# Performance work log

Hardware: AMD Instinct MI355X
Metric: run time of the kernel (lower is better)

## Reference

```python
import jax, jax.numpy as jnp
import numpy as np

N = 100000
E = 1600000
D_FEAT = 64
D_HID = 64
T = 20
DT = 0.5


def setup_inputs() -> dict:
    key = jax.random.key(0)
    ks = jax.random.split(key, 12)
    inp = {
        "S0": jax.random.uniform(ks[0], (N,), dtype=jnp.float32),
        "I0": jax.random.uniform(ks[1], (N,), dtype=jnp.float32),
        "R0": jnp.zeros((N,), dtype=jnp.float32),
        "time_grid": jnp.arange(T, dtype=jnp.float32),
        "node_feat": jax.random.normal(ks[2], (N, D_FEAT), dtype=jnp.float32),
        "edge_index": jax.random.randint(ks[3], (2, E), 0, N, dtype=jnp.int64),
        "edge_weight": jax.random.uniform(ks[4], (E,), dtype=jnp.float32),
        "W_msg": jax.random.normal(ks[5], (D_FEAT + 1, D_HID), dtype=jnp.float32) * 0.1,
        "W_self": jax.random.normal(ks[6], (D_FEAT + 1, D_HID), dtype=jnp.float32) * 0.1,
        "b_h": jnp.zeros((D_HID,), dtype=jnp.float32),
        "w_beta": jax.random.normal(ks[7], (D_HID,), dtype=jnp.float32) * 0.1,
        "b_beta": jnp.zeros((1,), dtype=jnp.float32),
        "w_gamma": jax.random.normal(ks[8], (D_HID,), dtype=jnp.float32) * 0.1,
        "b_gamma": jnp.zeros((1,), dtype=jnp.float32),
    }
    return inp


def reference(S0, I0, R0, time_grid, node_feat, edge_index, edge_weight,
              W_msg, W_self, b_h, w_beta, b_beta, w_gamma, b_gamma):
    n = S0.shape[0]
    src = edge_index[0]
    dst = edge_index[1]

    def step(carry, _):
        S, I, R = carry
        # gnn block: x_in = [node_feat, I]  -> [N, d_feat+1]
        x_in = jnp.concatenate([node_feat, I[:, None]], axis=-1)
        # project first, then gather: (x_in @ W_msg)[src] is math-equivalent to x_in[src] @ W_msg
        msg = (x_in @ W_msg)[src] * edge_weight[:, None]          # [E, d_hid]
        agg = jax.ops.segment_sum(msg, dst, num_segments=n)       # [N, d_hid]
        h = jax.nn.relu(agg + x_in @ W_self + b_h)
        # param net: per-node beta/gamma
        beta = jax.nn.sigmoid(h @ w_beta + b_beta[0])             # [N]
        gamma = jax.nn.sigmoid(h @ w_gamma + b_gamma[0])          # [N]
        # edge scatter-add force
        force = jax.ops.segment_sum(edge_weight * I[src], dst, num_segments=n)
        force = jnp.clip(force, 0.0, 1000.0)
        inf = beta * S * force
        rec = gamma * I
        S = jnp.clip(S + (-inf) * DT, 0.0, 1.0)
        I = jnp.clip(I + (inf - rec) * DT, 0.0, 1.0)
        R = jnp.clip(R + rec * DT, 0.0, 1.0)
        return (S, I, R), (I, beta, gamma)

    (_, _, _), (I_seq, betas, gammas) = jax.lax.scan(
        step, (S0, I0, R0), None, length=time_grid.shape[0])
    return I_seq, betas[-1], gammas[-1]
```

## Files before the change

### kernel.cpp

```cpp
#include <hip/hip_runtime.h>
#include <hip/hip_fp16.h>
#include <cstdint>
#include <cstddef>

#define DT_F 0.5f
#define ELL_C 64
#define NBIN 768
#define BCAP 512
#define NSC 96

__global__ void detect_i64(const long long* __restrict__ ei, int E, int n,
                           int* __restrict__ flag) {
    __shared__ int ok;
    if (threadIdx.x == 0) ok = 1;
    __syncthreads();
    int m = E < 2048 ? E : 2048;
    for (int i = threadIdx.x; i < m; i += blockDim.x) {
        long long v = ei[i];
        if (v < 0 || v >= (long long)n) ok = 0;
    }
    __syncthreads();
    if (threadIdx.x == 0) flag[0] = ok;
}

__device__ __forceinline__ int ld_idx(const void* ei, size_t pos, int w64) {
    return w64 ? (int)((const long long*)ei)[pos] : ((const int*)ei)[pos];
}

__global__ void k_bin(const void* __restrict__ ei, const float* __restrict__ ew,
                      const int* __restrict__ flag, int E, int n,
                      int colbits, float scale,
                      int2* __restrict__ staging, int scap,
                      int* __restrict__ gcur,
                      int* __restrict__ cnt, uint32_t* __restrict__ ev) {
    __shared__ int2 bins[8][BCAP];
    __shared__ int bcnt[8];
    __shared__ int gbase[8];
    int tid = threadIdx.x;
    if (tid < 8) bcnt[tid] = 0;
    __syncthreads();
    int per = (E + NBIN - 1) / NBIN;
    int e0 = blockIdx.x * per;
    int e1 = e0 + per; if (e1 > E) e1 = E;
    int w64 = flag[0];
    for (int e = e0 + tid; e < e1; e += blockDim.x) {
        int d = ld_idx(ei, (size_t)E + e, w64);
        uint32_t w15 = (uint32_t)(ew[e] * scale + 0.5f);
        uint32_t sw = (w15 << colbits) | (uint32_t)ld_idx(ei, e, w64);
        int s = (int)(((long long)d * 8) / n);
        int p = atomicAdd(&bcnt[s], 1);
        if (p < BCAP) {
            bins[s][p] = make_int2(d, (int)sw);
        } else {
            int q = atomicAdd(&cnt[d], 1);
            if (q < ELL_C) ev[(size_t)d * ELL_C + q] = sw;
        }
    }
    __syncthreads();
    if (tid < 8) {
        int c = bcnt[tid]; if (c > BCAP) c = BCAP;
        bcnt[tid] = c;
        gbase[tid] = atomicAdd(&gcur[tid], c);
    }
    __syncthreads();
    for (int s = 0; s < 8; ++s) {
        int c = bcnt[s], gb = gbase[s];
        for (int i = tid; i < c; i += blockDim.x) {
            int pos = gb + i;
            if (pos < scap) {
                staging[(size_t)s * scap + pos] = bins[s][i];
            } else {
                int2 t = bins[s][i];
                int q = atomicAdd(&cnt[t.x], 1);
                if (q < ELL_C) ev[(size_t)t.x * ELL_C + q] = (uint32_t)t.y;
            }
        }
    }
}

__global__ void k_scatter(const int2* __restrict__ staging, int scap,
                          const int* __restrict__ gcur,
                          int* __restrict__ cnt, uint32_t* __restrict__ ev) {
    int s   = blockIdx.x & 7;
    int blk = blockIdx.x >> 3;
    int tot = gcur[s]; if (tot > scap) tot = scap;
    int per = (tot + NSC - 1) / NSC;
    int i0 = blk * per;
    int i1 = i0 + per; if (i1 > tot) i1 = tot;
    for (int i = i0 + (int)threadIdx.x; i < i1; i += blockDim.x) {
        int2 t = staging[(size_t)s * scap + i];
        int p = atomicAdd(&cnt[t.x], 1);
        if (p < ELL_C) ev[(size_t)t.x * ELL_C + p] = (uint32_t)t.y;
    }
}

__global__ void k_h16(const float* __restrict__ x, __half* __restrict__ y, int n) {
    int i = blockIdx.x * blockDim.x + threadIdx.x;
    if (i < n) y[i] = __float2half(x[i]);
}

__global__ void proj_tiled(const float* __restrict__ nf,
                           const float* __restrict__ Wm,
                           const float* __restrict__ Wsf,
                           const float* __restrict__ bh,
                           __half* __restrict__ PMh, float* __restrict__ HC,
                           int n) {
    __shared__ float sWmT[64 * 65];
    __shared__ float sWsT[64 * 65];
    __shared__ float sNf[64 * 68];
    for (int i = threadIdx.x; i < 64 * 64; i += 256) {
        int k = i >> 6, j = i & 63;
        sWmT[j * 65 + k] = Wm[i];
        sWsT[j * 65 + k] = Wsf[i];
    }
    int node0 = blockIdx.x * 64;
    for (int i = threadIdx.x; i < 64 * 64; i += 256) {
        int r = i >> 6, c = i & 63;
        if (node0 + r < n) sNf[r * 68 + c] = nf[(size_t)(node0 + r) * 64 + c];
    }
    __syncthreads();
    int w   = threadIdx.x >> 6;
    int j   = threadIdx.x & 63;
    float accm[16], accs[16];
#pragma unroll
    for (int ni = 0; ni < 16; ++ni) { accm[ni] = 0.f; accs[ni] = 0.f; }
    for (int kq = 0; kq < 16; ++kq) {
        int k = kq * 4;
        float wm0 = sWmT[j * 65 + k],     wm1 = sWmT[j * 65 + k + 1];
        float wm2 = sWmT[j * 65 + k + 2], wm3 = sWmT[j * 65 + k + 3];
        float ws0 = sWsT[j * 65 + k],     ws1 = sWsT[j * 65 + k + 1];
        float ws2 = sWsT[j * 65 + k + 2], ws3 = sWsT[j * 65 + k + 3];
#pragma unroll
        for (int ni = 0; ni < 16; ++ni) {
            float4 a = *(const float4*)&sNf[(w * 16 + ni) * 68 + k];
            accm[ni] = fmaf(a.w, wm3, fmaf(a.z, wm2, fmaf(a.y, wm1, fmaf(a.x, wm0, accm[ni]))));
            accs[ni] = fmaf(a.w, ws3, fmaf(a.z, ws2, fmaf(a.y, ws1, fmaf(a.x, ws0, accs[ni]))));
        }
    }
    float bhl = bh[j];
#pragma unroll
    for (int ni = 0; ni < 16; ++ni) {
        int node = node0 + w * 16 + ni;
        if (node < n) {
            PMh[(size_t)node * 64 + j] = __float2half(accm[ni]);
            HC[(size_t)node * 64 + j] = accs[ni] + bhl;
        }
    }
}

__global__ void edge_wide_ell(const int* __restrict__ cnt,
                              const uint32_t* __restrict__ ev,
                              const __half* __restrict__ PMh,
                              const float* __restrict__ HCin,
                              __half* __restrict__ HCh, int n,
                              int colbits, float inv_scale) {
    int wave = (blockIdx.x * blockDim.x + threadIdx.x) >> 6;
    int lane = threadIdx.x & 63;
    if (wave >= n) return;
    uint32_t cmask = (1u << colbits) - 1;
    int deg = cnt[wave]; if (deg > ELL_C) deg = ELL_C;
    int d4 = deg & ~3;
    const uint32_t* row = ev + (size_t)wave * ELL_C;
    float acc0 = 0.f, acc1 = 0.f, acc2 = 0.f, acc3 = 0.f;
    for (int e = 0; e < d4; e += 4) {
        uint4 q = *(const uint4*)&row[e];
        float v0 = __half2float(PMh[(size_t)(q.x & cmask) * 64 + lane]);
        float v1 = __half2float(PMh[(size_t)(q.y & cmask) * 64 + lane]);
        float v2 = __half2float(PMh[(size_t)(q.z & cmask) * 64 + lane]);
        float v3 = __half2float(PMh[(size_t)(q.w & cmask) * 64 + lane]);
        acc0 = fmaf((float)(q.x >> colbits) * inv_scale, v0, acc0);
        acc1 = fmaf((float)(q.y >> colbits) * inv_scale, v1, acc1);
        acc2 = fmaf((float)(q.z >> colbits) * inv_scale, v2, acc2);
        acc3 = fmaf((float)(q.w >> colbits) * inv_scale, v3, acc3);
    }
    for (int e = d4; e < deg; ++e) {
        uint32_t q = row[e];
        acc0 = fmaf((float)(q >> colbits) * inv_scale,
                    __half2float(PMh[(size_t)(q & cmask) * 64 + lane]), acc0);
    }
    size_t o = (size_t)wave * 64 + lane;
    HCh[o] = __float2half(HCin[o] + ((acc0 + acc1) + (acc2 + acc3)));
}

__global__ void step_fused4(const int* __restrict__ cnt,
                            const uint32_t* __restrict__ ev,
                            const __half2* __restrict__ HCh2,
                            const float4* __restrict__ wmL4,
                            const float4* __restrict__ wsL4,
                            const float4* __restrict__ wb4, const float* __restrict__ bb,
                            const float4* __restrict__ wg4, const float* __restrict__ bg,
                            const float* __restrict__ I_old,
                            const __half* __restrict__ Ih_old,
                            __half* __restrict__ Ih_new,
                            float* __restrict__ S,
                            float* __restrict__ Iseq_t,
                            float* __restrict__ beta_out, float* __restrict__ gamma_out,
                            int n, int last, int colbits, float inv_scale) {
    int wid  = (blockIdx.x * blockDim.x + threadIdx.x) >> 6;
    int lane = threadIdx.x & 63;
    int l16  = lane & 15;
    int node = wid * 4 + (lane >> 4);
    if (node >= n) return;
    uint32_t cmask = (1u << colbits) - 1;
    int deg = cnt[node]; if (deg > ELL_C) deg = ELL_C;
    const uint32_t* row = ev + (size_t)node * ELL_C;
    float f = 0.f;
    for (int e = l16; e < deg; e += 16) {
        uint32_t p = row[e];
        f = fmaf((float)(p >> colbits) * inv_scale,
                 __half2float(Ih_old[p & cmask]), f);
    }
    f += __shfl_xor(f, 1); f += __shfl_xor(f, 2);
    f += __shfl_xor(f, 4); f += __shfl_xor(f, 8);
    float Iv = I_old[node];
    __half2 hA = HCh2[(size_t)node * 32 + l16 * 2];
    __half2 hB = HCh2[(size_t)node * 32 + l16 * 2 + 1];
    float2 fA = __half22float2(hA);
    float2 fB = __half22float2(hB);
    float4 wm = wmL4[l16], wsv = wsL4[l16];
    float4 h;
    h.x = fmaxf(fmaf(f, wm.x, fmaf(Iv, wsv.x, fA.x)), 0.f);
    h.y = fmaxf(fmaf(f, wm.y, fmaf(Iv, wsv.y, fA.y)), 0.f);
    h.z = fmaxf(fmaf(f, wm.z, fmaf(Iv, wsv.z, fB.x)), 0.f);
    h.w = fmaxf(fmaf(f, wm.w, fmaf(Iv, wsv.w, fB.y)), 0.f);
    float4 wbv = wb4[l16], wgv = wg4[l16];
    float pb = fmaf(h.x, wbv.x, fmaf(h.y, wbv.y, fmaf(h.z, wbv.z, h.w * wbv.w)));
    float pg = fmaf(h.x, wgv.x, fmaf(h.y, wgv.y, fmaf(h.z, wgv.z, h.w * wgv.w)));
    pb += __shfl_xor(pb, 1); pg += __shfl_xor(pg, 1);
    pb += __shfl_xor(pb, 2); pg += __shfl_xor(pg, 2);
    pb += __shfl_xor(pb, 4); pg += __shfl_xor(pg, 4);
    pb += __shfl_xor(pb, 8); pg += __shfl_xor(pg, 8);
    if (l16 == 0) {
        float beta  = 1.f / (1.f + expf(-(pb + bb[0])));
        float gamma = 1.f / (1.f + expf(-(pg + bg[0])));
        float fc = fminf(fmaxf(f, 0.f), 1000.f);
        float Sv = S[node];
        float inf_ = beta * Sv * fc;
        float rec  = gamma * Iv;
        float Sn = fminf(fmaxf(Sv - inf_ * DT_F, 0.f), 1.f);
        float In = fminf(fmaxf(Iv + (inf_ - rec) * DT_F, 0.f), 1.f);
        S[node] = Sn;
        Iseq_t[node] = In;
        Ih_new[node] = __float2half(In);
        if (last) { beta_out[node] = beta; gamma_out[node] = gamma; }
    }
}

extern "C" void kernel_launch(void* const* d_in, const int* in_sizes, int n_in,
                              void* d_out, int out_size, void* d_ws, size_t ws_size,
                              hipStream_t stream) {
    const float* S0  = (const float*)d_in[0];
    const float* I0  = (const float*)d_in[1];
    const float* nf  = (const float*)d_in[4];
    const void*  ei  = d_in[5];
    const float* ew  = (const float*)d_in[6];
    const float* Wm  = (const float*)d_in[7];
    const float* Wsf = (const float*)d_in[8];
    const float* bh  = (const float*)d_in[9];
    const float* wb  = (const float*)d_in[10];
    const float* bb  = (const float*)d_in[11];
    const float* wg  = (const float*)d_in[12];
    const float* bg  = (const float*)d_in[13];

    const int n = in_sizes[0];
    const int T = in_sizes[3];
    const int E = in_sizes[6];

    int colbits = 1;
    while ((1 << colbits) < n) ++colbits;
    float scale = (float)((1u << (32 - colbits)) - 1);
    float inv_scale = 1.0f / scale;
    const int scap = E / 4 + 65536;

    char* ws = (char*)d_ws;
    size_t off = 0;
    auto alloc = [&](size_t bytes) {
        size_t p = off;
        off = (off + bytes + 255) & ~(size_t)255;
        return p;
    };
    float*  HC      = (float*)(ws + alloc((size_t)n * 64 * 4));
    __half* PMh     = (__half*)(ws + alloc((size_t)n * 64 * 2));
    __half* HCh     = (__half*)(ws + alloc((size_t)n * 64 * 2));
    float*  S       = (float*)(ws + alloc((size_t)n * 4));
    __half* Ih0     = (__half*)(ws + alloc((size_t)n * 2));
    __half* IhA     = (__half*)(ws + alloc((size_t)n * 2));
    __half* IhB     = (__half*)(ws + alloc((size_t)n * 2));
    int*    cnt     = (int*)(ws + alloc((size_t)n * 4));
    uint32_t* ev    = (uint32_t*)(ws + alloc((size_t)n * ELL_C * 4));
    int2*   staging = (int2*)(ws + alloc((size_t)8 * scap * 8));
    int*    gcur    = (int*)(ws + alloc(256));
    int*    flag    = (int*)(ws + alloc(256));
    if (off > ws_size) return;

    float* out       = (float*)d_out;
    float* beta_out  = out + (size_t)T * n;
    float* gamma_out = out + (size_t)T * n + n;

    hipMemcpyAsync(S, S0, (size_t)n * 4, hipMemcpyDeviceToDevice, stream);
    hipMemsetAsync(cnt, 0, (size_t)n * 4, stream);
    hipMemsetAsync(gcur, 0, 256, stream);

    detect_i64<<<1, 256, 0, stream>>>((const long long*)ei, E, n, flag);
    k_bin<<<NBIN, 256, 0, stream>>>(ei, ew, flag, E, n, colbits, scale,
                                    staging, scap, gcur, cnt, ev);
    k_scatter<<<NSC * 8, 256, 0, stream>>>(staging, scap, gcur, cnt, ev);
    k_h16<<<(n + 255) / 256, 256, 0, stream>>>(I0, Ih0, n);

    proj_tiled<<<(n + 63) / 64, 256, 0, stream>>>(nf, Wm, Wsf, bh, PMh, HC, n);
    edge_wide_ell<<<(n * 64 + 255) / 256, 256, 0, stream>>>(
        cnt, ev, PMh, HC, HCh, n, colbits, inv_scale);

    const __half2* HCh2 = (const __half2*)HCh;
    const float4* wmL4 = (const float4*)(Wm  + 64 * 64);
    const float4* wsL4 = (const float4*)(Wsf + 64 * 64);
    const float4* wb4  = (const float4*)wb;
    const float4* wg4  = (const float4*)wg;
    int swaves = (n + 3) / 4;
    int sblocks = (swaves * 64 + 255) / 256;
    for (int t = 0; t < T; ++t) {
        const float*  Iold = (t == 0) ? I0 : out + (size_t)(t - 1) * n;
        const __half* Ihp  = (t == 0) ? Ih0 : ((t & 1) ? IhA : IhB);
        __half*       Ihc  = (t & 1) ? IhB : IhA;
        step_fused4<<<sblocks, 256, 0, stream>>>(
            cnt, ev, HCh2, wmL4, wsL4, wb4, bb, wg4, bg,
            Iold, Ihp, Ihc, S, out + (size_t)t * n, beta_out, gamma_out,
            n, t == T - 1 ? 1 : 0, colbits, inv_scale);
    }
}
```

Measured before the change: 503.5 us.

## Bucket edges into 512 destination ranges and build ELL rows in shared memory

Edge binning now partitions edges into 512 fine destination sub-ranges with small per-block LDS buckets. Each sub-range is then assembled into ELL rows with shared-memory atomics and written out coalesced, instead of using global atomics per edge. Overflow edges go to a separate list that a dedicated kernel processes. The projection kernel also drops its shared-memory tile of node features and reads them directly from global memory. This adds a kernel launch and an overflow path, and the order of entries within each ELL row may change.

```diff
diff --git a/kernel.cpp b/kernel.cpp
--- a/kernel.cpp
+++ b/kernel.cpp
@@ -5,9 +5,10 @@
 
 #define DT_F 0.5f
 #define ELL_C 64
-#define NBIN 768
-#define BCAP 512
-#define NSC 96
+#define NSUB 512
+#define LCAP 14
+#define NBIN 1024
+#define NLOC_MAX 208
 
 __global__ void detect_i64(const long long* __restrict__ ei, int E, int n,
                            int* __restrict__ flag) {
@@ -27,70 +28,104 @@
     return w64 ? (int)((const long long*)ei)[pos] : ((const int*)ei)[pos];
 }
 
-__global__ void k_bin(const void* __restrict__ ei, const float* __restrict__ ew,
-                      const int* __restrict__ flag, int E, int n,
-                      int colbits, float scale,
-                      int2* __restrict__ staging, int scap,
-                      int* __restrict__ gcur,
-                      int* __restrict__ cnt, uint32_t* __restrict__ ev) {
-    __shared__ int2 bins[8][BCAP];
-    __shared__ int bcnt[8];
-    __shared__ int gbase[8];
+__global__ void k_bin512(const void* __restrict__ ei, const float* __restrict__ ew,
+                         const int* __restrict__ flag, int E, int n,
+                         int colbits, float scale,
+                         int2* __restrict__ staging, int scap2,
+                         int* __restrict__ gcur,
+                         int2* __restrict__ ovf, int* __restrict__ ovcnt, int ovcap) {
+    __shared__ int2 bins[NSUB][LCAP];
+    __shared__ int bcnt[NSUB];
+    __shared__ int gbase[NSUB];
     int tid = threadIdx.x;
-    if (tid < 8) bcnt[tid] = 0;
+    for (int b = tid; b < NSUB; b += 256) bcnt[b] = 0;
     __syncthreads();
     int per = (E + NBIN - 1) / NBIN;
     int e0 = blockIdx.x * per;
     int e1 = e0 + per; if (e1 > E) e1 = E;
     int w64 = flag[0];
-    for (int e = e0 + tid; e < e1; e += blockDim.x) {
+    for (int e = e0 + tid; e < e1; e += 256) {
         int d = ld_idx(ei, (size_t)E + e, w64);
         uint32_t w15 = (uint32_t)(ew[e] * scale + 0.5f);
         uint32_t sw = (w15 << colbits) | (uint32_t)ld_idx(ei, e, w64);
-        int s = (int)(((long long)d * 8) / n);
-        int p = atomicAdd(&bcnt[s], 1);
-        if (p < BCAP) {
-            bins[s][p] = make_int2(d, (int)sw);
+        int sb = (int)(((long long)d * NSUB) / n);
+        int p = atomicAdd(&bcnt[sb], 1);
+        if (p < LCAP) {
+            bins[sb][p] = make_int2(d, (int)sw);
         } else {
-            int q = atomicAdd(&cnt[d], 1);
-            if (q < ELL_C) ev[(size_t)d * ELL_C + q] = sw;
-        }
-    }
-    __syncthreads();
-    if (tid < 8) {
-        int c = bcnt[tid]; if (c > BCAP) c = BCAP;
-        bcnt[tid] = c;
-        gbase[tid] = atomicAdd(&gcur[tid], c);
-    }
-    __syncthreads();
-    for (int s = 0; s < 8; ++s) {
-        int c = bcnt[s], gb = gbase[s];
-        for (int i = tid; i < c; i += blockDim.x) {
+            int q = atomicAdd(ovcnt, 1);
+            if (q < ovcap) ovf[q] = make_int2(d, (int)sw);
+        }
+    }
+    __syncthreads();
+    for (int b = tid; b < NSUB; b += 256) {
+        int c = bcnt[b]; if (c > LCAP) c = LCAP;
+        bcnt[b] = c;
+        gbase[b] = atomicAdd(&gcur[b], c);
+    }
+    __syncthreads();
+    for (int b = tid; b < NSUB; b += 256) {
+        int c = bcnt[b], gb = gbase[b];
+        for (int i = 0; i < c; ++i) {
             int pos = gb + i;
-            if (pos < scap) {
-                staging[(size_t)s * scap + pos] = bins[s][i];
+            if (pos < scap2) {
+                staging[(size_t)b * scap2 + pos] = bins[b][i];
             } else {
-                int2 t = bins[s][i];
-                int q = atomicAdd(&cnt[t.x], 1);
-                if (q < ELL_C) ev[(size_t)t.x * ELL_C + q] = (uint32_t)t.y;
+                int q = atomicAdd(ovcnt, 1);
+                if (q < ovcap) ovf[q] = bins[b][i];
             }
         }
     }
 }
 
-__global__ void k_scatter(const int2* __restrict__ staging, int scap,
-                          const int* __restrict__ gcur,
-                          int* __restrict__ cnt, uint32_t* __restrict__ ev) {
-    int s   = blockIdx.x & 7;
-    int blk = blockIdx.x >> 3;
-    int tot = gcur[s]; if (tot > scap) tot = scap;
-    int per = (tot + NSC - 1) / NSC;
-    int i0 = blk * per;
-    int i1 = i0 + per; if (i1 > tot) i1 = tot;
-    for (int i = i0 + (int)threadIdx.x; i < i1; i += blockDim.x) {
-        int2 t = staging[(size_t)s * scap + i];
+__global__ void k_scatter512(const int2* __restrict__ staging, int scap2,
+                             const int* __restrict__ gcur, int n,
+                             int* __restrict__ cnt, uint32_t* __restrict__ ev) {
+    __shared__ uint32_t lrow[NLOC_MAX * 64];
+    __shared__ int lcnt[NLOC_MAX];
+    int sb = blockIdx.x;
+    int lo = (int)(((long long)sb * n + NSUB - 1) / NSUB);
+    int hi = (int)(((long long)(sb + 1) * n + NSUB - 1) / NSUB);
+    if (hi > n) hi = n;
+    int nloc = hi - lo;
+    int tid = threadIdx.x;
+    int tot = gcur[sb]; if (tot > scap2) tot = scap2;
+    if (nloc <= NLOC_MAX) {
+        for (int i = tid; i < nloc; i += 256) lcnt[i] = 0;
+        __syncthreads();
+        for (int i = tid; i < tot; i += 256) {
+            int2 t = staging[(size_t)sb * scap2 + i];
+            int ni = t.x - lo;
+            int p = atomicAdd(&lcnt[ni], 1);
+            if (p < ELL_C) lrow[ni * 64 + p] = (uint32_t)t.y;
+        }
+        __syncthreads();
+        for (int idx = tid; idx < nloc * 64; idx += 256) {
+            int ni = idx >> 6, e = idx & 63;
+            int c = lcnt[ni]; if (c > ELL_C) c = ELL_C;
+            if (e < c) ev[(size_t)(lo + ni) * 64 + e] = lrow[idx];
+        }
+        for (int i = tid; i < nloc; i += 256) {
+            int c = lcnt[i]; if (c > ELL_C) c = ELL_C;
+            cnt[lo + i] = c;
+        }
+    } else {
+        for (int i = tid; i < tot; i += 256) {
+            int2 t = staging[(size_t)sb * scap2 + i];
+            int p = atomicAdd(&cnt[t.x], 1);
+            if (p < ELL_C) ev[(size_t)t.x * 64 + p] = (uint32_t)t.y;
+        }
+    }
+}
+
+__global__ void k_overflow(const int2* __restrict__ ovf, const int* __restrict__ ovcnt,
+                           int ovcap, int* __restrict__ cnt, uint32_t* __restrict__ ev) {
+    int tot = ovcnt[0]; if (tot > ovcap) tot = ovcap;
+    for (int i = blockIdx.x * blockDim.x + threadIdx.x; i < tot;
+         i += gridDim.x * blockDim.x) {
+        int2 t = ovf[i];
         int p = atomicAdd(&cnt[t.x], 1);
-        if (p < ELL_C) ev[(size_t)t.x * ELL_C + p] = (uint32_t)t.y;
+        if (p < ELL_C) ev[(size_t)t.x * 64 + p] = (uint32_t)t.y;
     }
 }
 
@@ -107,18 +142,13 @@
                            int n) {
     __shared__ float sWmT[64 * 65];
     __shared__ float sWsT[64 * 65];
-    __shared__ float sNf[64 * 68];
     for (int i = threadIdx.x; i < 64 * 64; i += 256) {
         int k = i >> 6, j = i & 63;
         sWmT[j * 65 + k] = Wm[i];
         sWsT[j * 65 + k] = Wsf[i];
     }
+    __syncthreads();
     int node0 = blockIdx.x * 64;
-    for (int i = threadIdx.x; i < 64 * 64; i += 256) {
-        int r = i >> 6, c = i & 63;
-        if (node0 + r < n) sNf[r * 68 + c] = nf[(size_t)(node0 + r) * 64 + c];
-    }
-    __syncthreads();
     int w   = threadIdx.x >> 6;
     int j   = threadIdx.x & 63;
     float accm[16], accs[16];
@@ -132,7 +162,9 @@
         float ws2 = sWsT[j * 65 + k + 2], ws3 = sWsT[j * 65 + k + 3];
 #pragma unroll
         for (int ni = 0; ni < 16; ++ni) {
-            float4 a = *(const float4*)&sNf[(w * 16 + ni) * 68 + k];
+            int node = node0 + w * 16 + ni;
+            float4 a = make_float4(0.f, 0.f, 0.f, 0.f);
+            if (node < n) a = *(const float4*)&nf[(size_t)node * 64 + k];
             accm[ni] = fmaf(a.w, wm3, fmaf(a.z, wm2, fmaf(a.y, wm1, fmaf(a.x, wm0, accm[ni]))));
             accs[ni] = fmaf(a.w, ws3, fmaf(a.z, ws2, fmaf(a.y, ws1, fmaf(a.x, ws0, accs[ni]))));
         }
@@ -270,7 +302,8 @@
     while ((1 << colbits) < n) ++colbits;
     float scale = (float)((1u << (32 - colbits)) - 1);
     float inv_scale = 1.0f / scale;
-    const int scap = E / 4 + 65536;
+    const int scap2 = E / NSUB + E / (NSUB * 4) + 256;
+    const int ovcap = E;
 
     char* ws = (char*)d_ws;
     size_t off = 0;
@@ -288,8 +321,10 @@
     __half* IhB     = (__half*)(ws + alloc((size_t)n * 2));
     int*    cnt     = (int*)(ws + alloc((size_t)n * 4));
     uint32_t* ev    = (uint32_t*)(ws + alloc((size_t)n * ELL_C * 4));
-    int2*   staging = (int2*)(ws + alloc((size_t)8 * scap * 8));
-    int*    gcur    = (int*)(ws + alloc(256));
+    int2*   staging = (int2*)(ws + alloc((size_t)NSUB * scap2 * 8));
+    int2*   ovf     = (int2*)(ws + alloc((size_t)ovcap * 8));
+    int*    gcur    = (int*)(ws + alloc((size_t)NSUB * 4));
+    int*    ovcnt   = (int*)(ws + alloc(256));
     int*    flag    = (int*)(ws + alloc(256));
     if (off > ws_size) return;
 
@@ -299,12 +334,14 @@
 
     hipMemcpyAsync(S, S0, (size_t)n * 4, hipMemcpyDeviceToDevice, stream);
     hipMemsetAsync(cnt, 0, (size_t)n * 4, stream);
-    hipMemsetAsync(gcur, 0, 256, stream);
+    hipMemsetAsync(gcur, 0, (size_t)NSUB * 4, stream);
+    hipMemsetAsync(ovcnt, 0, 256, stream);
 
     detect_i64<<<1, 256, 0, stream>>>((const long long*)ei, E, n, flag);
-    k_bin<<<NBIN, 256, 0, stream>>>(ei, ew, flag, E, n, colbits, scale,
-                                    staging, scap, gcur, cnt, ev);
-    k_scatter<<<NSC * 8, 256, 0, stream>>>(staging, scap, gcur, cnt, ev);
+    k_bin512<<<NBIN, 256, 0, stream>>>(ei, ew, flag, E, n, colbits, scale,
+                                       staging, scap2, gcur, ovf, ovcnt, ovcap);
+    k_scatter512<<<NSUB, 256, 0, stream>>>(staging, scap2, gcur, n, cnt, ev);
+    k_overflow<<<64, 256, 0, stream>>>(ovf, ovcnt, ovcap, cnt, ev);
     k_h16<<<(n + 255) / 256, 256, 0, stream>>>(I0, Ih0, n);
 
     proj_tiled<<<(n + 63) / 64, 256, 0, stream>>>(nf, Wm, Wsf, bh, PMh, HC, n);
```

New measurement: 477.7 us. 5.1% less time.
